# Kernel tuning notes

Hardware: AMD Instinct MI355X
Metric: run time of the kernel (lower is better)

Reference implementation:

```python
import jax, jax.numpy as jnp
import numpy as np

N = 50000          # nodes
E = 800000         # directed edges
F_IN = 64          # input feature dim
H = 64             # GCN hidden dim
DH = 32            # decoder hidden dim


def setup_inputs() -> dict:
    key = jax.random.key(0)
    ks = jax.random.split(key, 10)
    x = jax.random.normal(ks[0], (N, F_IN), dtype=jnp.float32)
    edge_index = jax.random.randint(ks[1], (2, E), 0, N, dtype=jnp.int64)
    s = 0.1  # weight init scale
    return {
        "x": x,
        "edge_index": edge_index,
        "W1": jax.random.normal(ks[2], (F_IN, H), dtype=jnp.float32) * s,
        "b1": jnp.zeros((H,), dtype=jnp.float32),
        "W2": jax.random.normal(ks[3], (H, H), dtype=jnp.float32) * s,
        "b2": jnp.zeros((H,), dtype=jnp.float32),
        "Wd1": jax.random.normal(ks[4], (H, DH), dtype=jnp.float32) * s,
        "bd1": jnp.zeros((DH,), dtype=jnp.float32),
        "Wd2": jax.random.normal(ks[5], (DH, 1), dtype=jnp.float32) * s,
        "bd2": jnp.zeros((1,), dtype=jnp.float32),
    }


def _gcn_conv(x, src, dst, norm, W, b, n):
    # transform then gather-scale-scatter (PyG GCNConv message passing)
    h = x @ W                                   # (n, out)
    msg = h[src] * norm[:, None]                # (E+n, out) gather on src
    out = jax.ops.segment_sum(msg, dst, num_segments=n)  # scatter-add on dst
    return out + b


def reference(x, edge_index, W1, b1, W2, b2, Wd1, bd1, Wd2, bd2):
    n = x.shape[0]
    # add self-loops (GCNConv default)
    loops = jnp.arange(n, dtype=edge_index.dtype)
    src = jnp.concatenate([edge_index[0], loops])
    dst = jnp.concatenate([edge_index[1], loops])
    # symmetric normalization D^{-1/2} A D^{-1/2}, degree on dst incl. self-loops
    deg = jax.ops.segment_sum(jnp.ones_like(dst, dtype=x.dtype), dst, num_segments=n)
    dinv = jnp.where(deg > 0, deg ** -0.5, 0.0)
    norm = dinv[src] * dinv[dst]                # (E+n,)
    h = jax.nn.relu(_gcn_conv(x, src, dst, norm, W1, b1, n))
    # gcn_dropout is identity in eval mode
    h = jax.nn.relu(_gcn_conv(h, src, dst, norm, W2, b2, n))
    h = jax.nn.relu(h @ Wd1 + bd1)              # decoder MLP
    pred = (h @ Wd2 + bd2).squeeze(-1)          # (N,)
    return pred
```

## Files before the change

### kernel.cpp

```cpp
#include <hip/hip_runtime.h>

#define NF 64

__device__ __forceinline__ float rlf(float v, int l) {
    return __int_as_float(__builtin_amdgcn_readlane(__float_as_int(v), l));
}


__global__ void count_deg(const int* __restrict__ dst, int* __restrict__ cnt, int E) {
    int e = blockIdx.x * blockDim.x + threadIdx.x;
    if (e < E) atomicAdd(&cnt[dst[e]], 1);
}

__global__ __launch_bounds__(1024) void scan_blk(const int* __restrict__ cnt,
                                                 int* __restrict__ rowptr,
                                                 int* __restrict__ bsum, int n) {
    __shared__ int wsum[16];
    __shared__ int wexcl[16];
    int tid = threadIdx.x, lane = tid & 63, w = tid >> 6;
    int i = blockIdx.x * 1024 + tid;
    int v = (i < n) ? cnt[i] : 0;
    int inc = v;
#pragma unroll
    for (int d = 1; d < 64; d <<= 1) {
        int t = __shfl_up(inc, d);
        if (lane >= d) inc += t;
    }
    if (lane == 63) wsum[w] = inc;
    __syncthreads();
    if (w == 0 && lane < 16) {
        int s = wsum[lane];
        int e2 = s;
#pragma unroll
        for (int d = 1; d < 16; d <<= 1) {
            int t = __shfl_up(e2, d);
            if (lane >= d) e2 += t;
        }
        wexcl[lane] = e2 - s;
    }
    __syncthreads();
    if (i < n) rowptr[i] = wexcl[w] + inc - v;
    if (tid == 1023) bsum[blockIdx.x] = wexcl[15] + wsum[15];
}

__global__ __launch_bounds__(1024) void scan_part(int* __restrict__ bsum, int nb) {
    __shared__ int wsum[16];
    __shared__ int wexcl[16];
    int tid = threadIdx.x, lane = tid & 63, w = tid >> 6;
    int v = (tid < nb) ? bsum[tid] : 0;
    int inc = v;
#pragma unroll
    for (int d = 1; d < 64; d <<= 1) {
        int t = __shfl_up(inc, d);
        if (lane >= d) inc += t;
    }
    if (lane == 63) wsum[w] = inc;
    __syncthreads();
    if (w == 0 && lane < 16) {
        int s = wsum[lane];
        int e2 = s;
#pragma unroll
        for (int d = 1; d < 16; d <<= 1) {
            int t = __shfl_up(e2, d);
            if (lane >= d) e2 += t;
        }
        wexcl[lane] = e2 - s;
    }
    __syncthreads();
    if (tid < nb) bsum[tid] = wexcl[w] + inc - v;
}

__global__ void scan_add(int* __restrict__ rowptr, const int* __restrict__ bsum,
                         const int* __restrict__ cnt, float* __restrict__ dinv,
                         int* __restrict__ fill, int n) {
    int i = blockIdx.x * blockDim.x + threadIdx.x;
    if (i < n) {
        int c = cnt[i];
        int r = rowptr[i] + bsum[i >> 10];
        rowptr[i] = r;
        if (i == n - 1) rowptr[n] = r + c;
        dinv[i] = rsqrtf((float)(c + 1));
        fill[i] = 0;
    }
}

__global__ void fill_csr(const int* __restrict__ src, const int* __restrict__ dst,
                         const int* __restrict__ rowptr, int* __restrict__ fill,
                         const float* __restrict__ dinv, int2* __restrict__ pairs, int E) {
    int e = blockIdx.x * blockDim.x + threadIdx.x;
    if (e >= E) return;
    int d = dst[e], s = src[e];
    int pos = rowptr[d] + atomicAdd(&fill[d], 1);
    pairs[pos] = make_int2(s, __float_as_int(dinv[s]));
}


template <bool DEC>
__global__ __launch_bounds__(256) void gcn_layer(
    const int2* __restrict__ pairs, const int* __restrict__ rowptr,
    const float* __restrict__ dinv, const float* __restrict__ xin,
    const float* __restrict__ W, const float* __restrict__ bias,
    float* __restrict__ xout,
    const float* __restrict__ Wd1, const float* __restrict__ bd1,
    const float* __restrict__ Wd2, const float* __restrict__ bd2,
    float* __restrict__ pred, int n)
{
    __shared__ float Wd1l[64][32];
    __shared__ float bd1l[32];
    __shared__ float w2l[32];
    int tid = threadIdx.x;
    int lane = tid & 63;
    if (DEC) {
        for (int i = tid; i < 2048; i += 256) Wd1l[i >> 5][i & 31] = Wd1[i];
        if (tid < 32) { bd1l[tid] = bd1[tid]; w2l[tid] = Wd2[tid]; }
    }
    __syncthreads();

    float wcol[64];
#pragma unroll
    for (int k = 0; k < 64; ++k) wcol[k] = W[k * NF + lane];
    float bv = bias[lane];
    float bd2v = DEC ? bd2[0] : 0.0f;

    int q = lane >> 4;
    int fl = (lane & 15) * 4;

    int wid = blockIdx.x * 4 + (tid >> 6);
    int nw = gridDim.x * 4;
    for (int i = wid; i < n; i += nw) {
        float di = dinv[i];
        int jb = __builtin_amdgcn_readfirstlane(rowptr[i]);
        int je = __builtin_amdgcn_readfirstlane(rowptr[i + 1]);

        float4 sv = *reinterpret_cast<const float4*>(xin + (size_t)i * NF + fl);
        float wself = (q == 0) ? di * di : 0.0f;
        float a[4];
        a[0] = sv.x * wself; a[1] = sv.y * wself;
        a[2] = sv.z * wself; a[3] = sv.w * wself;

        for (int base = jb; base < je; base += 64) {
            int cnt = min(64, je - base);
            int2 p = make_int2(0, 0);
            if (base + lane < je) p = pairs[base + lane];
            for (int e = 0; e < cnt; e += 4) {
                int sl = e + q;
                int s = __shfl(p.x, sl);
                float wgt = __int_as_float(__shfl(p.y, sl)) * di;
                float4 v = *reinterpret_cast<const float4*>(xin + (size_t)s * NF + fl);
                a[0] = fmaf(v.x, wgt, a[0]);
                a[1] = fmaf(v.y, wgt, a[1]);
                a[2] = fmaf(v.z, wgt, a[2]);
                a[3] = fmaf(v.w, wgt, a[3]);
            }
        }
#pragma unroll
        for (int j = 0; j < 4; ++j) {
            a[j] += __shfl_xor(a[j], 16);
            a[j] += __shfl_xor(a[j], 32);
        }

        float o = bv;
#pragma unroll
        for (int k = 0; k < 64; ++k) o = fmaf(rlf(a[k & 3], k >> 2), wcol[k], o);
        o = fmaxf(o, 0.0f);

        if (!DEC) {
            xout[(size_t)i * NF + lane] = o;
        } else {
            int j = lane & 31;
            float s = 0.0f;
#pragma unroll
            for (int k = 0; k < 64; ++k) s = fmaf(rlf(o, k), Wd1l[k][j], s);
            float hj = fmaxf(s + bd1l[j], 0.0f);
            float pp = hj * w2l[j];
#pragma unroll
            for (int m = 16; m >= 1; m >>= 1) pp += __shfl_xor(pp, m);
            if (lane == 0) pred[i] = pp + bd2v;
        }
    }
}


extern "C" void kernel_launch(void* const* d_in, const int* in_sizes, int n_in,
                              void* d_out, int out_size, void* d_ws, size_t ws_size,
                              hipStream_t stream) {
    const float* x   = (const float*)d_in[0];
    const int*   ei  = (const int*)d_in[1];
    const float* W1  = (const float*)d_in[2];
    const float* b1  = (const float*)d_in[3];
    const float* W2  = (const float*)d_in[4];
    const float* b2  = (const float*)d_in[5];
    const float* Wd1 = (const float*)d_in[6];
    const float* bd1 = (const float*)d_in[7];
    const float* Wd2 = (const float*)d_in[8];
    const float* bd2 = (const float*)d_in[9];
    float* pred = (float*)d_out;

    const int N = in_sizes[0] / NF;
    const int E = in_sizes[1] / 2;
    const int* src = ei;
    const int* dst = ei + E;

    char* ws = (char*)d_ws;
    size_t off = 0;
    int*   cnt    = (int*)(ws + off);   off += (size_t)4 * N;
    int*   rowptr = (int*)(ws + off);   off += (size_t)4 * (N + 1);
    int*   fill   = (int*)(ws + off);   off += (size_t)4 * N;
    float* dinv   = (float*)(ws + off); off += (size_t)4 * N;
    int*   bsum   = (int*)(ws + off);   off += (size_t)4 * 1024;
    off = (off + 15) & ~(size_t)15;
    int2*  pairs  = (int2*)(ws + off);  off += (size_t)8 * E;
    float* h1     = (float*)(ws + off);

    const int B = 256;
    const int eb = (E + B - 1) / B;
    const int nb = (N + B - 1) / B;
    const int nb1024 = (N + 1023) / 1024;

    hipMemsetAsync(cnt, 0, (size_t)4 * N, stream);
    count_deg<<<eb, B, 0, stream>>>(dst, cnt, E);
    scan_blk<<<nb1024, 1024, 0, stream>>>(cnt, rowptr, bsum, N);
    scan_part<<<1, 1024, 0, stream>>>(bsum, nb1024);
    scan_add<<<nb, B, 0, stream>>>(rowptr, bsum, cnt, dinv, fill, N);
    fill_csr<<<eb, B, 0, stream>>>(src, dst, rowptr, fill, dinv, pairs, E);

    const int gb = 1536;

    gcn_layer<false><<<gb, B, 0, stream>>>(pairs, rowptr, dinv, x, W1, b1, h1,
                                           Wd1, bd1, Wd2, bd2, pred, N);
    gcn_layer<true><<<gb, B, 0, stream>>>(pairs, rowptr, dinv, h1, W2, b2, h1,
                                          Wd1, bd1, Wd2, bd2, pred, N);
}
```

Measured before the change: 280.4 us.

## Process two nodes per wavefront and store only source indices in CSR

Each wavefront now aggregates two adjacent nodes at once. This interleaves two independent gather streams so more memory loads are in flight, and the W-column loads are shared by both nodes. The CSR stores only source indices instead of (src, dinv) pairs, which halves the edge-list footprint; dinv[src] is gathered inside the layer kernel instead. The transform and decoder reductions are split into several partial accumulators to shorten dependency chains, and the grid is reduced to 1024 blocks. In exchange there are more registers and extra gathers, and load imbalance grows because the loop runs to the longer of the two rows.

New measurement: 285.9 us. Within noise of the previous version (+2.0%).

```diff
diff --git a/kernel.cpp b/kernel.cpp
--- a/kernel.cpp
+++ b/kernel.cpp
@@ -5,6 +5,7 @@
 __device__ __forceinline__ float rlf(float v, int l) {
     return __int_as_float(__builtin_amdgcn_readlane(__float_as_int(v), l));
 }
+__device__ __forceinline__ int rfl(int v) { return __builtin_amdgcn_readfirstlane(v); }
 
 
 __global__ void count_deg(const int* __restrict__ dst, int* __restrict__ cnt, int E) {
@@ -86,18 +87,18 @@
 
 __global__ void fill_csr(const int* __restrict__ src, const int* __restrict__ dst,
                          const int* __restrict__ rowptr, int* __restrict__ fill,
-                         const float* __restrict__ dinv, int2* __restrict__ pairs, int E) {
+                         int* __restrict__ srcs, int E) {
     int e = blockIdx.x * blockDim.x + threadIdx.x;
     if (e >= E) return;
-    int d = dst[e], s = src[e];
+    int d = dst[e];
     int pos = rowptr[d] + atomicAdd(&fill[d], 1);
-    pairs[pos] = make_int2(s, __float_as_int(dinv[s]));
+    srcs[pos] = src[e];
 }
 
 
 template <bool DEC>
 __global__ __launch_bounds__(256) void gcn_layer(
-    const int2* __restrict__ pairs, const int* __restrict__ rowptr,
+    const int* __restrict__ srcs, const int* __restrict__ rowptr,
     const float* __restrict__ dinv, const float* __restrict__ xin,
     const float* __restrict__ W, const float* __restrict__ bias,
     float* __restrict__ xout,
@@ -125,57 +126,106 @@
     int q = lane >> 4;
     int fl = (lane & 15) * 4;
 
-    int wid = blockIdx.x * 4 + (tid >> 6);
+    int widx = blockIdx.x * 4 + (tid >> 6);
     int nw = gridDim.x * 4;
-    for (int i = wid; i < n; i += nw) {
-        float di = dinv[i];
-        int jb = __builtin_amdgcn_readfirstlane(rowptr[i]);
-        int je = __builtin_amdgcn_readfirstlane(rowptr[i + 1]);
-
-        float4 sv = *reinterpret_cast<const float4*>(xin + (size_t)i * NF + fl);
-        float wself = (q == 0) ? di * di : 0.0f;
-        float a[4];
-        a[0] = sv.x * wself; a[1] = sv.y * wself;
-        a[2] = sv.z * wself; a[3] = sv.w * wself;
-
-        for (int base = jb; base < je; base += 64) {
-            int cnt = min(64, je - base);
-            int2 p = make_int2(0, 0);
-            if (base + lane < je) p = pairs[base + lane];
-            for (int e = 0; e < cnt; e += 4) {
+    int npair = (n + 1) >> 1;
+    for (int t = widx; t < npair; t += nw) {
+        int i0 = t * 2, i1 = i0 + 1;
+        bool has1 = i1 < n;
+        float d0 = dinv[i0];
+        float d1 = has1 ? dinv[i1] : 0.0f;
+        int jb0 = rfl(rowptr[i0]);
+        int je0 = rfl(rowptr[i0 + 1]);
+        int je1 = has1 ? rfl(rowptr[i0 + 2]) : je0;
+        int jb1 = je0;
+
+        float4 sv0 = *reinterpret_cast<const float4*>(xin + (size_t)i0 * NF + fl);
+        float4 sv1 = *reinterpret_cast<const float4*>(xin + (size_t)(has1 ? i1 : i0) * NF + fl);
+        float ws0 = (q == 0) ? d0 * d0 : 0.0f;
+        float ws1 = (q == 0) ? d1 * d1 : 0.0f;
+        float a0[4] = {sv0.x * ws0, sv0.y * ws0, sv0.z * ws0, sv0.w * ws0};
+        float a1[4] = {sv1.x * ws1, sv1.y * ws1, sv1.z * ws1, sv1.w * ws1};
+
+        int base0 = jb0, base1 = jb1;
+        int rem0 = je0 - jb0, rem1 = je1 - jb1;
+        while (rem0 > 0 || rem1 > 0) {
+            int c0 = min(64, rem0), c1 = min(64, rem1);
+            int s0 = 0, s1 = 0;
+            float w0 = 0.0f, w1 = 0.0f;
+            if (lane < c0) { s0 = srcs[base0 + lane]; w0 = dinv[s0] * d0; }
+            if (lane < c1) { s1 = srcs[base1 + lane]; w1 = dinv[s1] * d1; }
+            int cmax = max(c0, c1);
+            for (int e = 0; e < cmax; e += 4) {
                 int sl = e + q;
-                int s = __shfl(p.x, sl);
-                float wgt = __int_as_float(__shfl(p.y, sl)) * di;
-                float4 v = *reinterpret_cast<const float4*>(xin + (size_t)s * NF + fl);
-                a[0] = fmaf(v.x, wgt, a[0]);
-                a[1] = fmaf(v.y, wgt, a[1]);
-                a[2] = fmaf(v.z, wgt, a[2]);
-                a[3] = fmaf(v.w, wgt, a[3]);
-            }
-        }
-#pragma unroll
-        for (int j = 0; j < 4; ++j) {
-            a[j] += __shfl_xor(a[j], 16);
-            a[j] += __shfl_xor(a[j], 32);
-        }
-
-        float o = bv;
-#pragma unroll
-        for (int k = 0; k < 64; ++k) o = fmaf(rlf(a[k & 3], k >> 2), wcol[k], o);
-        o = fmaxf(o, 0.0f);
+                int   sA = __shfl(s0, sl);
+                float wA = __shfl(w0, sl);
+                int   sB = __shfl(s1, sl);
+                float wB = __shfl(w1, sl);
+                float4 vA = *reinterpret_cast<const float4*>(xin + (size_t)sA * NF + fl);
+                float4 vB = *reinterpret_cast<const float4*>(xin + (size_t)sB * NF + fl);
+                a0[0] = fmaf(vA.x, wA, a0[0]);
+                a0[1] = fmaf(vA.y, wA, a0[1]);
+                a0[2] = fmaf(vA.z, wA, a0[2]);
+                a0[3] = fmaf(vA.w, wA, a0[3]);
+                a1[0] = fmaf(vB.x, wB, a1[0]);
+                a1[1] = fmaf(vB.y, wB, a1[1]);
+                a1[2] = fmaf(vB.z, wB, a1[2]);
+                a1[3] = fmaf(vB.w, wB, a1[3]);
+            }
+            base0 += 64; base1 += 64; rem0 -= 64; rem1 -= 64;
+        }
+#pragma unroll
+        for (int j2 = 0; j2 < 4; ++j2) {
+            a0[j2] += __shfl_xor(a0[j2], 16);
+            a0[j2] += __shfl_xor(a0[j2], 32);
+            a1[j2] += __shfl_xor(a1[j2], 16);
+            a1[j2] += __shfl_xor(a1[j2], 32);
+        }
+
+        float t00 = 0, t01 = 0, t02 = 0, t03 = 0;
+        float t10 = 0, t11 = 0, t12 = 0, t13 = 0;
+#pragma unroll
+        for (int m = 0; m < 16; ++m) {
+            float wc0 = wcol[4 * m], wc1 = wcol[4 * m + 1];
+            float wc2 = wcol[4 * m + 2], wc3 = wcol[4 * m + 3];
+            t00 = fmaf(rlf(a0[0], m), wc0, t00);
+            t01 = fmaf(rlf(a0[1], m), wc1, t01);
+            t02 = fmaf(rlf(a0[2], m), wc2, t02);
+            t03 = fmaf(rlf(a0[3], m), wc3, t03);
+            t10 = fmaf(rlf(a1[0], m), wc0, t10);
+            t11 = fmaf(rlf(a1[1], m), wc1, t11);
+            t12 = fmaf(rlf(a1[2], m), wc2, t12);
+            t13 = fmaf(rlf(a1[3], m), wc3, t13);
+        }
+        float o0 = fmaxf(((t00 + t01) + (t02 + t03)) + bv, 0.0f);
+        float o1 = fmaxf(((t10 + t11) + (t12 + t13)) + bv, 0.0f);
 
         if (!DEC) {
-            xout[(size_t)i * NF + lane] = o;
+            xout[(size_t)i0 * NF + lane] = o0;
+            if (has1) xout[(size_t)i1 * NF + lane] = o1;
         } else {
             int j = lane & 31;
-            float s = 0.0f;
-#pragma unroll
-            for (int k = 0; k < 64; ++k) s = fmaf(rlf(o, k), Wd1l[k][j], s);
-            float hj = fmaxf(s + bd1l[j], 0.0f);
-            float pp = hj * w2l[j];
-#pragma unroll
-            for (int m = 16; m >= 1; m >>= 1) pp += __shfl_xor(pp, m);
-            if (lane == 0) pred[i] = pp + bd2v;
+            float sA = 0, sB = 0, sC = 0, sD = 0;
+#pragma unroll
+            for (int k = 0; k < 64; k += 2) {
+                float wd0 = Wd1l[k][j], wd1 = Wd1l[k + 1][j];
+                sA = fmaf(rlf(o0, k), wd0, sA);
+                sB = fmaf(rlf(o0, k + 1), wd1, sB);
+                sC = fmaf(rlf(o1, k), wd0, sC);
+                sD = fmaf(rlf(o1, k + 1), wd1, sD);
+            }
+            float h0 = fmaxf(sA + sB + bd1l[j], 0.0f);
+            float h1 = fmaxf(sC + sD + bd1l[j], 0.0f);
+            float p0 = h0 * w2l[j], p1 = h1 * w2l[j];
+#pragma unroll
+            for (int m = 16; m >= 1; m >>= 1) {
+                p0 += __shfl_xor(p0, m);
+                p1 += __shfl_xor(p1, m);
+            }
+            if (lane == 0) {
+                pred[i0] = p0 + bd2v;
+                if (has1) pred[i1] = p1 + bd2v;
+            }
         }
     }
 }
@@ -209,7 +259,8 @@
     float* dinv   = (float*)(ws + off); off += (size_t)4 * N;
     int*   bsum   = (int*)(ws + off);   off += (size_t)4 * 1024;
     off = (off + 15) & ~(size_t)15;
-    int2*  pairs  = (int2*)(ws + off);  off += (size_t)8 * E;
+    int*   srcs   = (int*)(ws + off);   off += (size_t)4 * E;
+    off = (off + 15) & ~(size_t)15;
     float* h1     = (float*)(ws + off);
 
     const int B = 256;
@@ -222,12 +273,12 @@
     scan_blk<<<nb1024, 1024, 0, stream>>>(cnt, rowptr, bsum, N);
     scan_part<<<1, 1024, 0, stream>>>(bsum, nb1024);
     scan_add<<<nb, B, 0, stream>>>(rowptr, bsum, cnt, dinv, fill, N);
-    fill_csr<<<eb, B, 0, stream>>>(src, dst, rowptr, fill, dinv, pairs, E);
-
-    const int gb = 1536;
-
-    gcn_layer<false><<<gb, B, 0, stream>>>(pairs, rowptr, dinv, x, W1, b1, h1,
+    fill_csr<<<eb, B, 0, stream>>>(src, dst, rowptr, fill, srcs, E);
+
+    const int gb = 1024;
+
+    gcn_layer<false><<<gb, B, 0, stream>>>(srcs, rowptr, dinv, x, W1, b1, h1,
                                            Wd1, bd1, Wd2, bd2, pred, N);
-    gcn_layer<true><<<gb, B, 0, stream>>>(pairs, rowptr, dinv, h1, W2, b2, h1,
+    gcn_layer<true><<<gb, B, 0, stream>>>(srcs, rowptr, dinv, h1, W2, b2, h1,
                                           Wd1, bd1, Wd2, bd2, pred, N);
 }
```

## Prefetch next node's CSR bounds and edge chunk; split FMA accumulation chains

Applied to the files above, without the earlier changes.

Software-pipelines the node loop so each wave loads the next node's rowptr bounds and first 64 edge pairs while it aggregates the current node, hiding that dependent-load latency. The per-edge multiply by di is moved out of the inner loop and applied once after the cross-lane reduction. The 64-term transform and decoder dot products are split into independent partial accumulators to shorten FMA dependency chains. Launch bounds now request 6 blocks per SM, which may force register spilling because of the 64-entry wcol array plus the prefetch registers.

Result: slower. 496.0 us (+76.9%).

```diff
diff --git a/kernel.cpp b/kernel.cpp
--- a/kernel.cpp
+++ b/kernel.cpp
@@ -5,6 +5,7 @@
 __device__ __forceinline__ float rlf(float v, int l) {
     return __int_as_float(__builtin_amdgcn_readlane(__float_as_int(v), l));
 }
+__device__ __forceinline__ int rfl(int v) { return __builtin_amdgcn_readfirstlane(v); }
 
 
 __global__ void count_deg(const int* __restrict__ dst, int* __restrict__ cnt, int E) {
@@ -96,7 +97,7 @@
 
 
 template <bool DEC>
-__global__ __launch_bounds__(256) void gcn_layer(
+__global__ __launch_bounds__(256, 6) void gcn_layer(
     const int2* __restrict__ pairs, const int* __restrict__ rowptr,
     const float* __restrict__ dinv, const float* __restrict__ xin,
     const float* __restrict__ W, const float* __restrict__ bias,
@@ -127,25 +128,38 @@
 
     int wid = blockIdx.x * 4 + (tid >> 6);
     int nw = gridDim.x * 4;
-    for (int i = wid; i < n; i += nw) {
+
+    int i = wid;
+    int jb = 0, je = 0;
+    int2 p = make_int2(0, 0);
+    if (i < n) {
+        jb = rfl(rowptr[i]);
+        je = rfl(rowptr[i + 1]);
+        if (jb + lane < je) p = pairs[jb + lane];
+    }
+
+    for (; i < n; i += nw) {
+        int inext = i + nw;
+        int jbN = 0, jeN = 0;
+        int2 pN = make_int2(0, 0);
+        if (inext < n) {
+            jbN = rfl(rowptr[inext]);
+            jeN = rfl(rowptr[inext + 1]);
+            if (jbN + lane < jeN) pN = pairs[jbN + lane];
+        }
+
         float di = dinv[i];
-        int jb = __builtin_amdgcn_readfirstlane(rowptr[i]);
-        int je = __builtin_amdgcn_readfirstlane(rowptr[i + 1]);
-
         float4 sv = *reinterpret_cast<const float4*>(xin + (size_t)i * NF + fl);
-        float wself = (q == 0) ? di * di : 0.0f;
-        float a[4];
-        a[0] = sv.x * wself; a[1] = sv.y * wself;
-        a[2] = sv.z * wself; a[3] = sv.w * wself;
-
-        for (int base = jb; base < je; base += 64) {
-            int cnt = min(64, je - base);
-            int2 p = make_int2(0, 0);
-            if (base + lane < je) p = pairs[base + lane];
-            for (int e = 0; e < cnt; e += 4) {
+        float ws = (q == 0) ? di : 0.0f;
+        float a[4] = {sv.x * ws, sv.y * ws, sv.z * ws, sv.w * ws};
+
+        int deg = je - jb;
+        {
+            int c0 = min(64, deg);
+            for (int e = 0; e < c0; e += 4) {
                 int sl = e + q;
-                int s = __shfl(p.x, sl);
-                float wgt = __int_as_float(__shfl(p.y, sl)) * di;
+                int   s = __shfl(p.x, sl);
+                float wgt = __int_as_float(__shfl(p.y, sl));
                 float4 v = *reinterpret_cast<const float4*>(xin + (size_t)s * NF + fl);
                 a[0] = fmaf(v.x, wgt, a[0]);
                 a[1] = fmaf(v.y, wgt, a[1]);
@@ -153,30 +167,56 @@
                 a[3] = fmaf(v.w, wgt, a[3]);
             }
         }
-#pragma unroll
-        for (int j = 0; j < 4; ++j) {
-            a[j] += __shfl_xor(a[j], 16);
-            a[j] += __shfl_xor(a[j], 32);
-        }
-
-        float o = bv;
-#pragma unroll
-        for (int k = 0; k < 64; ++k) o = fmaf(rlf(a[k & 3], k >> 2), wcol[k], o);
-        o = fmaxf(o, 0.0f);
+        for (int base = jb + 64; base < je; base += 64) {
+            int c = min(64, je - base);
+            int2 p2 = make_int2(0, 0);
+            if (base + lane < je) p2 = pairs[base + lane];
+            for (int e = 0; e < c; e += 4) {
+                int sl = e + q;
+                int   s = __shfl(p2.x, sl);
+                float wgt = __int_as_float(__shfl(p2.y, sl));
+                float4 v = *reinterpret_cast<const float4*>(xin + (size_t)s * NF + fl);
+                a[0] = fmaf(v.x, wgt, a[0]);
+                a[1] = fmaf(v.y, wgt, a[1]);
+                a[2] = fmaf(v.z, wgt, a[2]);
+                a[3] = fmaf(v.w, wgt, a[3]);
+            }
+        }
+#pragma unroll
+        for (int j2 = 0; j2 < 4; ++j2) {
+            a[j2] += __shfl_xor(a[j2], 16);
+            a[j2] += __shfl_xor(a[j2], 32);
+            a[j2] *= di;
+        }
+
+        float t0 = 0, t1 = 0, t2 = 0, t3 = 0;
+#pragma unroll
+        for (int m = 0; m < 16; ++m) {
+            t0 = fmaf(rlf(a[0], m), wcol[4 * m + 0], t0);
+            t1 = fmaf(rlf(a[1], m), wcol[4 * m + 1], t1);
+            t2 = fmaf(rlf(a[2], m), wcol[4 * m + 2], t2);
+            t3 = fmaf(rlf(a[3], m), wcol[4 * m + 3], t3);
+        }
+        float o = fmaxf((t0 + t1) + (t2 + t3) + bv, 0.0f);
 
         if (!DEC) {
             xout[(size_t)i * NF + lane] = o;
         } else {
             int j = lane & 31;
-            float s = 0.0f;
-#pragma unroll
-            for (int k = 0; k < 64; ++k) s = fmaf(rlf(o, k), Wd1l[k][j], s);
-            float hj = fmaxf(s + bd1l[j], 0.0f);
+            float sA = 0, sB = 0;
+#pragma unroll
+            for (int k = 0; k < 64; k += 2) {
+                sA = fmaf(rlf(o, k), Wd1l[k][j], sA);
+                sB = fmaf(rlf(o, k + 1), Wd1l[k + 1][j], sB);
+            }
+            float hj = fmaxf(sA + sB + bd1l[j], 0.0f);
             float pp = hj * w2l[j];
 #pragma unroll
             for (int m = 16; m >= 1; m >>= 1) pp += __shfl_xor(pp, m);
             if (lane == 0) pred[i] = pp + bd2v;
         }
+
+        p = pN; jb = jbN; je = jeN;
     }
 }
 
```
